# Optimization experiments

Hardware: AMD Instinct MI355X
Metric: run time of the kernel (lower is better)

Reference implementation:

```python
import jax, jax.numpy as jnp
import numpy as np

B, L, HID, H = 2, 2048, 1024, 16
HD = HID // H
MAX_REL = 2


def setup_inputs() -> dict:
    key = jax.random.key(0)
    ks = jax.random.split(key, 16)
    s = 0.02
    return {
        "query": jax.random.normal(ks[0], (B, L, HID), jnp.float32),
        "key": jax.random.normal(ks[1], (B, L, HID), jnp.float32),
        "value": jax.random.normal(ks[2], (B, L, HID), jnp.float32),
        "Wq": jax.random.normal(ks[3], (HID, HID), jnp.float32) * s,
        "bq": jnp.zeros((HID,), jnp.float32),
        "Wk": jax.random.normal(ks[4], (HID, HID), jnp.float32) * s,
        "bk": jnp.zeros((HID,), jnp.float32),
        "Wv": jax.random.normal(ks[5], (HID, HID), jnp.float32) * s,
        "bv": jnp.zeros((HID,), jnp.float32),
        "Wo": jax.random.normal(ks[6], (HID, HID), jnp.float32) * s,
        "bo": jnp.zeros((HID,), jnp.float32),
        "rel_k_table": jax.random.normal(ks[7], (2 * MAX_REL + 1, HD), jnp.float32) * s,
        "rel_v_table": jax.random.normal(ks[8], (2 * MAX_REL + 1, HD), jnp.float32) * s,
    }


def _rel_embeddings(table, len_q, len_k):
    # Shaw-style clipped relative position lookup -> [len_q, len_k, head_dim]
    dist = jnp.arange(len_k)[None, :] - jnp.arange(len_q)[:, None]
    idx = jnp.clip(dist, -MAX_REL, MAX_REL) + MAX_REL
    return table[idx]


def reference(query, key, value, Wq, bq, Wk, bk, Wv, bv, Wo, bo, rel_k_table, rel_v_table):
    b, lq, hid = query.shape
    lk = key.shape[1]
    q = (query @ Wq.T + bq).reshape(b, lq, H, HD)   # [b, lq, h, hd]
    k = (key @ Wk.T + bk).reshape(b, lk, H, HD)     # [b, lk, h, hd]
    v = (value @ Wv.T + bv).reshape(b, lk, H, HD)   # [b, lk, h, hd]

    rk = _rel_embeddings(rel_k_table, lq, lk)       # [lq, lk, hd]
    rv = _rel_embeddings(rel_v_table, lq, lk)       # [lq, lk, hd]

    attn1 = jnp.einsum('bqhd,bkhd->bhqk', q, k)
    attn2 = jnp.einsum('bqhd,qkd->bhqk', q, rk)
    # NOTE: original code averages the two scores and does NOT divide by sqrt(head_dim)
    attn = jax.nn.softmax((attn1 + attn2) * 0.5, axis=-1)

    w1 = jnp.einsum('bhqk,bkhd->bhqd', attn, v)
    w2 = jnp.einsum('bhqk,qkd->bhqd', attn, rv)
    x = (w1 + w2).transpose(0, 2, 1, 3).reshape(b, lq, hid)
    return x @ Wo.T + bo
```

## Files before the change

kernel.cpp:

```cpp
#include <hip/hip_runtime.h>
#include <hip/hip_bf16.h>
#include <math.h>

typedef __attribute__((ext_vector_type(8))) short bf16x8;
typedef __attribute__((ext_vector_type(4))) float f32x4;
typedef __attribute__((ext_vector_type(16))) float f32x16;

constexpr int Bc   = 2;
constexpr int Lc   = 2048;
constexpr int HIDc = 1024;
constexpr int Hc   = 16;
constexpr int HDc  = 64;
constexpr int Mc   = 4096;

__device__ __forceinline__ ushort f2bf(float f) {
  uint u = __float_as_uint(f);
  u += 0x7fff + ((u >> 16) & 1);
  return (ushort)(u >> 16);
}

__device__ __forceinline__ void gload16(const ushort* g, ushort* l) {
  __builtin_amdgcn_global_load_lds(
      (const __attribute__((address_space(1))) uint*)(const void*)g,
      (__attribute__((address_space(3))) uint*)(void*)l, 16, 0, 0);
}

__device__ __forceinline__ uint cvtpk(float lo, float hi_) {
  uint r;
  asm("v_cvt_pk_bf16_f32 %0, %1, %2" : "=v"(r) : "v"(lo), "v"(hi_));
  return r;
}
__device__ __forceinline__ void pswap(uint &a, uint &b) {
  asm("v_permlane32_swap_b32 %0, %1" : "+v"(a), "+v"(b));
}

template<int MODE>
__device__ __forceinline__ void gemm_core(
    const float* __restrict__ A, const float* __restrict__ Bw,
    const float* __restrict__ bias, float* __restrict__ Cf,
    ushort* __restrict__ Cb, int tile,
    ushort (*As)[2048], ushort (*Bs)[4096])
{
  const int tid  = threadIdx.x;
  const int lane = tid & 63;
  const int w    = tid >> 6;
  const int g    = lane >> 4;
  const int lc   = lane & 15;
  const int wr   = w >> 2;
  const int wc   = w & 3;
  const int row0 = (tile >> 3) * 64;
  const int col0 = (tile & 7) * 128;

  const int sr  = tid >> 2;
  const int sc_ = tid & 3;
  const int wofs = sr*32 + (sc_ ^ ((sr >> 1) & 3))*8;
  const float* pA = A  + (size_t)(row0 + sr) * HIDc + sc_*8;
  const float* pB = Bw + (size_t)(col0 + sr) * HIDc + sc_*8;

  int aoff[2], boff[2];
  #pragma unroll
  for (int mi = 0; mi < 2; ++mi) {
    int r = wr*32 + mi*16 + lc;
    aoff[mi] = r*32 + (g ^ ((r >> 1) & 3)) * 8;
  }
  #pragma unroll
  for (int ni = 0; ni < 2; ++ni) {
    int r = wc*32 + ni*16 + lc;
    boff[ni] = r*32 + (g ^ ((r >> 1) & 3)) * 8;
  }

  f32x4 acc[2][2];
  #pragma unroll
  for (int mi = 0; mi < 2; ++mi)
    #pragma unroll
    for (int ni = 0; ni < 2; ++ni) acc[mi][ni] = (f32x4){0.f,0.f,0.f,0.f};

  float4 a0, a1, b0, b1;
  auto ld = [&](int ko) {
    b0 = *(const float4*)(pB + ko);
    b1 = *(const float4*)(pB + ko + 4);
    if (tid < 256) {
      a0 = *(const float4*)(pA + ko);
      a1 = *(const float4*)(pA + ko + 4);
    }
  };
  auto wrbuf = [&](int bi) {
    ushort tb[8] = { f2bf(b0.x), f2bf(b0.y), f2bf(b0.z), f2bf(b0.w),
                     f2bf(b1.x), f2bf(b1.y), f2bf(b1.z), f2bf(b1.w) };
    *(uint4*)&Bs[bi][wofs] = *(uint4*)tb;
    if (tid < 256) {
      ushort ta[8] = { f2bf(a0.x), f2bf(a0.y), f2bf(a0.z), f2bf(a0.w),
                       f2bf(a1.x), f2bf(a1.y), f2bf(a1.z), f2bf(a1.w) };
      *(uint4*)&As[bi][wofs] = *(uint4*)ta;
    }
  };

  ld(0); wrbuf(0);
  __syncthreads();

  for (int t = 0; t < 32; ++t) {
    if (t < 31) ld((t + 1) * 32);
    const ushort* as = As[t & 1];
    const ushort* bs = Bs[t & 1];
    bf16x8 af[2], bfr[2];
    #pragma unroll
    for (int mi = 0; mi < 2; ++mi) af[mi] = *(const bf16x8*)&as[aoff[mi]];
    #pragma unroll
    for (int ni = 0; ni < 2; ++ni) bfr[ni] = *(const bf16x8*)&bs[boff[ni]];
    #pragma unroll
    for (int mi = 0; mi < 2; ++mi)
      #pragma unroll
      for (int ni = 0; ni < 2; ++ni)
        acc[mi][ni] = __builtin_amdgcn_mfma_f32_16x16x32_bf16(af[mi], bfr[ni], acc[mi][ni], 0, 0, 0);
    if (t < 31) wrbuf((t + 1) & 1);
    __syncthreads();
  }

  const int colbase = col0 + wc*32;
  if (MODE == 0) {
    #pragma unroll
    for (int mi = 0; mi < 2; ++mi) {
      int row = row0 + wr*32 + mi*16 + 4*g;
      #pragma unroll
      for (int ni = 0; ni < 2; ++ni) {
        int col = colbase + ni*16 + lc;
        float bb = bias[col];
        #pragma unroll
        for (int reg = 0; reg < 4; ++reg)
          Cf[(size_t)(row + reg) * HIDc + col] = acc[mi][ni][reg] + bb;
      }
    }
  } else if (MODE == 1) {
    #pragma unroll
    for (int mi = 0; mi < 2; ++mi) {
      int row = row0 + wr*32 + mi*16 + 4*g;
      int b = row >> 11, qq = row & 2047;
      #pragma unroll
      for (int ni = 0; ni < 2; ++ni) {
        int col = colbase + ni*16 + lc;
        int h = col >> 6, d = col & 63;
        float bb = bias[col];
        size_t base = (((size_t)b*Hc + h)*Lc + qq)*HDc + d;
        #pragma unroll
        for (int reg = 0; reg < 4; ++reg)
          Cb[base + (size_t)reg*HDc] = f2bf(acc[mi][ni][reg] + bb);
      }
    }
  } else {
    #pragma unroll
    for (int mi = 0; mi < 2; ++mi) {
      int row = row0 + wr*32 + mi*16 + 4*g;
      int b = row >> 11, kk = row & 2047;
      #pragma unroll
      for (int ni = 0; ni < 2; ++ni) {
        int col = colbase + ni*16 + lc;
        int h = col >> 6, d = col & 63;
        float bb = bias[col];
        ushort t4[4];
        #pragma unroll
        for (int reg = 0; reg < 4; ++reg) t4[reg] = f2bf(acc[mi][ni][reg] + bb);
        *(uint2*)&Cb[(((size_t)b*Hc + h)*HDc + d)*Lc + kk] = *(uint2*)t4;
      }
    }
  }
}

__global__ __launch_bounds__(512)
void gemm_fused(const float* __restrict__ q, const float* __restrict__ k,
                const float* __restrict__ v,
                const float* __restrict__ Wq, const float* __restrict__ Wk,
                const float* __restrict__ Wv,
                const float* __restrict__ bq, const float* __restrict__ bk,
                const float* __restrict__ bv,
                ushort* Qc, ushort* Kc, ushort* Vt)
{
  __shared__ ushort As[2][2048];
  __shared__ ushort Bs[2][4096];
  int gi   = blockIdx.x >> 9;
  int tile = blockIdx.x & 511;
  if (gi == 0)      gemm_core<1>(q, Wq, bq, nullptr, Qc, tile, As, Bs);
  else if (gi == 1) gemm_core<1>(k, Wk, bk, nullptr, Kc, tile, As, Bs);
  else              gemm_core<2>(v, Wv, bv, nullptr, Vt, tile, As, Bs);
}

__global__ __launch_bounds__(512)
void gemm_out(const float* __restrict__ X, const float* __restrict__ Wo,
              const float* __restrict__ bo, float* __restrict__ out)
{
  __shared__ ushort As[2][2048];
  __shared__ ushort Bs[2][4096];
  gemm_core<0>(X, Wo, bo, out, nullptr, blockIdx.x, As, Bs);
}

__global__ __launch_bounds__(128)
void attn_mfma32(const ushort* __restrict__ Qc, const ushort* __restrict__ Kc,
                 const ushort* __restrict__ Vt, const float* __restrict__ relk,
                 const float* __restrict__ relv, float* __restrict__ X)
{
  __shared__ ushort KVs[2][4608];

  const int tid  = threadIdx.x;
  const int w    = tid >> 6;
  const int lane = tid & 63;
  const int lq   = lane & 31;
  const int hi   = lane >> 5;

  const int swz  = (blockIdx.x & 7) * 128 + (blockIdx.x >> 3);
  const int qblk = swz & 31;
  const int bh   = swz >> 5;
  const int b    = bh >> 4;
  const int h    = bh & 15;
  const int qw   = qblk*64 + w*32;
  const int qabs = qw + lq;

  constexpr float C2 = 0.72134752f;

  const ushort* Kbh = Kc + (size_t)bh*Lc*HDc;
  const ushort* Vbh = Vt + (size_t)bh*HDc*Lc;

  bf16x8 qf[4];
  const ushort* qbase = Qc + ((size_t)bh*Lc + qabs)*HDc + 8*hi;
  #pragma unroll
  for (int s = 0; s < 4; ++s) qf[s] = *(const bf16x8*)(qbase + 16*s);

  f32x16 dc;
  #pragma unroll
  for (int i = 0; i < 16; ++i) dc[i] = 0.f;
  #pragma unroll
  for (int s = 0; s < 4; ++s) {
    union { ushort u[8]; bf16x8 v; } rf;
    #pragma unroll
    for (int j = 0; j < 8; ++j) rf.u[j] = 0;
    if (lq < 5) {
      #pragma unroll
      for (int j = 0; j < 8; ++j) rf.u[j] = f2bf(relk[lq*HDc + 16*s + 8*hi + j]);
    }
    dc = __builtin_amdgcn_mfma_f32_32x32x16_bf16(rf.v, qf[s], dc, 0, 0, 0);
  }
  float o0 = __shfl_xor(dc[0], 32), o1 = __shfl_xor(dc[1], 32),
        o2 = __shfl_xor(dc[2], 32), o3 = __shfl_xor(dc[3], 32);
  float dqh0, dqh1, dqh2, dqh3, dqh4;
  if (hi == 0) { dqh0 = dc[0]; dqh1 = dc[1]; dqh2 = dc[2]; dqh3 = dc[3]; dqh4 = o0; }
  else         { dqh0 = o0;    dqh1 = o1;    dqh2 = o2;    dqh3 = o3;    dqh4 = dc[0]; }
  dqh0 *= C2; dqh1 *= C2; dqh2 *= C2; dqh3 *= C2; dqh4 *= C2;

  f32x16 acc0, acc1;
  #pragma unroll
  for (int i = 0; i < 16; ++i) { acc0[i] = 0.f; acc1[i] = 0.f; }
  float lsum = 0.f, llo = 0.f, e1 = 0.f, e2 = 0.f, e3 = 0.f;

  auto stage = [&](ushort* dst, int k0) {
    #pragma unroll
    for (int seg = 0; seg < 5; ++seg) {
      int widx = seg*2 + w;
      if (widx < 5) {
        int vc = widx*64 + lane;
        int row = vc/5, ch = vc - row*5;
        gload16(Vbh + (size_t)row*Lc + k0 + ch*8, dst + vc*8);
      } else if (widx < 9) {
        int kc = (widx - 5)*64 + lane;
        int row = kc >> 3, pch = kc & 7;
        int gch = pch ^ (row & 7);
        gload16(Kbh + (size_t)(k0 + row)*HDc + gch*8, dst + (320 + kc)*8);
      }
    }
  };

  stage(KVs[0], 0);
  __syncthreads();

  for (int t = 0; t < Lc/32; ++t) {
    const ushort* vb_ = KVs[t & 1];
    const ushort* kb_ = vb_ + 2560;
    if (t + 1 < Lc/32) stage(KVs[(t+1) & 1], (t+1)*32);
    const int kb = t*32;

    bf16x8 kfa[4];
    #pragma unroll
    for (int s = 0; s < 4; ++s)
      kfa[s] = *(const bf16x8*)&kb_[lq*64 + ((2*s + hi) ^ (lq & 7))*8];
    f32x16 c0;
    #pragma unroll
    for (int i = 0; i < 16; ++i) c0[i] = 0.f;
    __builtin_amdgcn_s_setprio(1);
    #pragma unroll
    for (int s = 0; s < 4; ++s)
      c0 = __builtin_amdgcn_mfma_f32_32x32x16_bf16(kfa[s], qf[s], c0, 0, 0, 0);
    __builtin_amdgcn_s_setprio(0);

    bf16x8 vf00 = *(const bf16x8*)&vb_[lq*40      + hi*8];
    bf16x8 vf01 = *(const bf16x8*)&vb_[(32+lq)*40 + hi*8];
    bf16x8 vf10 = *(const bf16x8*)&vb_[lq*40      + (2+hi)*8];
    bf16x8 vf11 = *(const bf16x8*)&vb_[(32+lq)*40 + (2+hi)*8];

    uint pk[8];
    const bool allhi = (kb >= qw + 33);
    const bool alllo = (kb + 33 <= qw);
    if (allhi | alllo) {
      const float dq = allhi ? dqh4 : dqh0;
      float gs = 0.f;
      #pragma unroll
      for (int jj = 0; jj < 8; ++jj) {
        float pa = __builtin_amdgcn_exp2f(__builtin_fmaf(c0[2*jj],   C2, dq));
        float pb = __builtin_amdgcn_exp2f(__builtin_fmaf(c0[2*jj+1], C2, dq));
        gs += pa + pb;
        pk[jj] = cvtpk(pa, pb);
      }
      lsum += gs;
      if (alllo) llo += gs;
    } else {
      int bnum = kb + 4*hi - qabs;
      #pragma unroll
      for (int jj = 0; jj < 8; ++jj) {
        int r0 = 2*jj;
        int d0 = bnum + ((r0 & 3) + 8*(r0 >> 2));
        int d1 = d0 + 1;
        float dqa = d0 <= -2 ? dqh0 : (d0 >= 2 ? dqh4 :
                    (d0 == -1 ? dqh1 : (d0 == 0 ? dqh2 : dqh3)));
        float dqb = d1 <= -2 ? dqh0 : (d1 >= 2 ? dqh4 :
                    (d1 == -1 ? dqh1 : (d1 == 0 ? dqh2 : dqh3)));
        float pa = __builtin_amdgcn_exp2f(__builtin_fmaf(c0[r0],   C2, dqa));
        float pb = __builtin_amdgcn_exp2f(__builtin_fmaf(c0[r0+1], C2, dqb));
        lsum += pa + pb;
        llo += (d0 <= -2 ? pa : 0.f) + (d1 <= -2 ? pb : 0.f);
        e1  += (d0 == -1 ? pa : 0.f) + (d1 == -1 ? pb : 0.f);
        e2  += (d0 ==  0 ? pa : 0.f) + (d1 ==  0 ? pb : 0.f);
        e3  += (d0 ==  1 ? pa : 0.f) + (d1 ==  1 ? pb : 0.f);
        pk[jj] = cvtpk(pa, pb);
      }
    }

    uint X0 = pk[0], X1 = pk[1], Y0 = pk[2], Y1 = pk[3];
    pswap(X0, Y0); pswap(X1, Y1);
    union { uint u[4]; bf16x8 v; } aw0;
    aw0.u[0] = X0; aw0.u[1] = X1; aw0.u[2] = Y0; aw0.u[3] = Y1;
    X0 = pk[4]; X1 = pk[5]; Y0 = pk[6]; Y1 = pk[7];
    pswap(X0, Y0); pswap(X1, Y1);
    union { uint u[4]; bf16x8 v; } aw1;
    aw1.u[0] = X0; aw1.u[1] = X1; aw1.u[2] = Y0; aw1.u[3] = Y1;
    __builtin_amdgcn_s_setprio(1);
    acc0 = __builtin_amdgcn_mfma_f32_32x32x16_bf16(aw0.v, vf00, acc0, 0, 0, 0);
    acc1 = __builtin_amdgcn_mfma_f32_32x32x16_bf16(aw0.v, vf01, acc1, 0, 0, 0);
    acc0 = __builtin_amdgcn_mfma_f32_32x32x16_bf16(aw1.v, vf10, acc0, 0, 0, 0);
    acc1 = __builtin_amdgcn_mfma_f32_32x32x16_bf16(aw1.v, vf11, acc1, 0, 0, 0);
    __builtin_amdgcn_s_setprio(0);
    __syncthreads();
  }

  float Ls = lsum + __shfl_xor(lsum, 32);
  float Lo = llo  + __shfl_xor(llo, 32);
  float E1 = e1   + __shfl_xor(e1, 32);
  float E2 = e2   + __shfl_xor(e2, 32);
  float E3 = e3   + __shfl_xor(e3, 32);
  float inv = 1.f / Ls;
  float s0v = Lo*inv, s1v = E1*inv, s2v = E2*inv, s3v = E3*inv;
  float s4v = 1.f - s0v - s1v - s2v - s3v;

  float rvv[5][2];
  #pragma unroll
  for (int r = 0; r < 5; ++r) {
    rvv[r][0] = relv[r*HDc + lq];
    rvv[r][1] = relv[r*HDc + 32 + lq];
  }
  #pragma unroll
  for (int r = 0; r < 16; ++r) {
    int qloc = ((r & 3) + 8*(r >> 2)) + 4*hi;
    float iv = __shfl(inv, qloc);
    float t0 = __shfl(s0v, qloc);
    float t1 = __shfl(s1v, qloc);
    float t2 = __shfl(s2v, qloc);
    float t3 = __shfl(s3v, qloc);
    float t4 = __shfl(s4v, qloc);
    size_t rowb = ((size_t)(b*Lc + qw + qloc))*HIDc + h*HDc;
    X[rowb + lq]      = acc0[r]*iv + t0*rvv[0][0] + t1*rvv[1][0] + t2*rvv[2][0]
                      + t3*rvv[3][0] + t4*rvv[4][0];
    X[rowb + 32 + lq] = acc1[r]*iv + t0*rvv[0][1] + t1*rvv[1][1] + t2*rvv[2][1]
                      + t3*rvv[3][1] + t4*rvv[4][1];
  }
}

extern "C" void kernel_launch(void* const* d_in, const int* in_sizes, int n_in,
                              void* d_out, int out_size, void* d_ws, size_t ws_size,
                              hipStream_t stream) {
  const float* query = (const float*)d_in[0];
  const float* key   = (const float*)d_in[1];
  const float* value = (const float*)d_in[2];
  const float* Wq    = (const float*)d_in[3];
  const float* bq    = (const float*)d_in[4];
  const float* Wk    = (const float*)d_in[5];
  const float* bk    = (const float*)d_in[6];
  const float* Wv    = (const float*)d_in[7];
  const float* bv    = (const float*)d_in[8];
  const float* Wo    = (const float*)d_in[9];
  const float* bo    = (const float*)d_in[10];
  const float* relk  = (const float*)d_in[11];
  const float* relv  = (const float*)d_in[12];
  float* out = (float*)d_out;

  size_t S = (size_t)Bc * Hc * Lc * HDc;
  ushort* Qc = (ushort*)d_ws;
  ushort* Kc = Qc + S;
  ushort* Vt = Kc + S;
  float*  Xb = (float*)(Vt + S);

  gemm_fused<<<3*512, 512, 0, stream>>>(query, key, value, Wq, Wk, Wv,
                                        bq, bk, bv, Qc, Kc, Vt);

  attn_mfma32<<<Bc * Hc * (Lc / 64), 128, 0, stream>>>(Qc, Kc, Vt, relk, relv, Xb);

  gemm_out<<<512, 512, 0, stream>>>(Xb, Wo, bo, out);
}
```

Before: 178.4 us.

## Process two 32-row query groups per wave to reuse K/V tiles

Each wave in the attention kernel now handles 64 query rows as two 32-row groups, so the block covers 128 queries and the grid halves to 512 blocks. Every K/V tile staged in LDS and loaded into registers is reused by both groups. This halves global K/V traffic and LDS reads per query and gives more MFMA work per barrier. The cost is doubled accumulator and softmax-state registers, which may lower occupancy, and fewer blocks to spread across CUs.

```diff
diff --git a/kernel.cpp b/kernel.cpp
--- a/kernel.cpp
+++ b/kernel.cpp
@@ -205,27 +205,27 @@
   const int lq   = lane & 31;
   const int hi   = lane >> 5;
 
-  const int swz  = (blockIdx.x & 7) * 128 + (blockIdx.x >> 3);
-  const int qblk = swz & 31;
-  const int bh   = swz >> 5;
+  const int swz  = (blockIdx.x & 7) * 64 + (blockIdx.x >> 3);
+  const int qblk = swz & 15;
+  const int bh   = swz >> 4;
   const int b    = bh >> 4;
   const int h    = bh & 15;
-  const int qw   = qblk*64 + w*32;
-  const int qabs = qw + lq;
+  const int qw   = qblk*128 + w*64;
 
   constexpr float C2 = 0.72134752f;
 
   const ushort* Kbh = Kc + (size_t)bh*Lc*HDc;
   const ushort* Vbh = Vt + (size_t)bh*HDc*Lc;
 
-  bf16x8 qf[4];
-  const ushort* qbase = Qc + ((size_t)bh*Lc + qabs)*HDc + 8*hi;
-  #pragma unroll
-  for (int s = 0; s < 4; ++s) qf[s] = *(const bf16x8*)(qbase + 16*s);
-
-  f32x16 dc;
-  #pragma unroll
-  for (int i = 0; i < 16; ++i) dc[i] = 0.f;
+  bf16x8 qf[2][4];
+  #pragma unroll
+  for (int g = 0; g < 2; ++g) {
+    const ushort* qbase = Qc + ((size_t)bh*Lc + qw + 32*g + lq)*HDc + 8*hi;
+    #pragma unroll
+    for (int s = 0; s < 4; ++s) qf[g][s] = *(const bf16x8*)(qbase + 16*s);
+  }
+
+  bf16x8 rkf[4];
   #pragma unroll
   for (int s = 0; s < 4; ++s) {
     union { ushort u[8]; bf16x8 v; } rf;
@@ -235,19 +235,36 @@
       #pragma unroll
       for (int j = 0; j < 8; ++j) rf.u[j] = f2bf(relk[lq*HDc + 16*s + 8*hi + j]);
     }
-    dc = __builtin_amdgcn_mfma_f32_32x32x16_bf16(rf.v, qf[s], dc, 0, 0, 0);
-  }
-  float o0 = __shfl_xor(dc[0], 32), o1 = __shfl_xor(dc[1], 32),
-        o2 = __shfl_xor(dc[2], 32), o3 = __shfl_xor(dc[3], 32);
-  float dqh0, dqh1, dqh2, dqh3, dqh4;
-  if (hi == 0) { dqh0 = dc[0]; dqh1 = dc[1]; dqh2 = dc[2]; dqh3 = dc[3]; dqh4 = o0; }
-  else         { dqh0 = o0;    dqh1 = o1;    dqh2 = o2;    dqh3 = o3;    dqh4 = dc[0]; }
-  dqh0 *= C2; dqh1 *= C2; dqh2 *= C2; dqh3 *= C2; dqh4 *= C2;
-
-  f32x16 acc0, acc1;
-  #pragma unroll
-  for (int i = 0; i < 16; ++i) { acc0[i] = 0.f; acc1[i] = 0.f; }
-  float lsum = 0.f, llo = 0.f, e1 = 0.f, e2 = 0.f, e3 = 0.f;
+    rkf[s] = rf.v;
+  }
+
+  float dqh[2][5];
+  #pragma unroll
+  for (int g = 0; g < 2; ++g) {
+    f32x16 dc;
+    #pragma unroll
+    for (int i = 0; i < 16; ++i) dc[i] = 0.f;
+    #pragma unroll
+    for (int s = 0; s < 4; ++s)
+      dc = __builtin_amdgcn_mfma_f32_32x32x16_bf16(rkf[s], qf[g][s], dc, 0, 0, 0);
+    float o0 = __shfl_xor(dc[0], 32), o1 = __shfl_xor(dc[1], 32),
+          o2 = __shfl_xor(dc[2], 32), o3 = __shfl_xor(dc[3], 32);
+    if (hi == 0) { dqh[g][0] = dc[0]; dqh[g][1] = dc[1]; dqh[g][2] = dc[2];
+                   dqh[g][3] = dc[3]; dqh[g][4] = o0; }
+    else         { dqh[g][0] = o0;    dqh[g][1] = o1;    dqh[g][2] = o2;
+                   dqh[g][3] = o3;    dqh[g][4] = dc[0]; }
+    #pragma unroll
+    for (int r = 0; r < 5; ++r) dqh[g][r] *= C2;
+  }
+
+  f32x16 acc0[2], acc1[2];
+  float lsum[2], llo[2], e1[2], e2[2], e3[2];
+  #pragma unroll
+  for (int g = 0; g < 2; ++g) {
+    #pragma unroll
+    for (int i = 0; i < 16; ++i) { acc0[g][i] = 0.f; acc1[g][i] = 0.f; }
+    lsum[g] = llo[g] = e1[g] = e2[g] = e3[g] = 0.f;
+  }
 
   auto stage = [&](ushort* dst, int k0) {
     #pragma unroll
@@ -279,82 +296,78 @@
     #pragma unroll
     for (int s = 0; s < 4; ++s)
       kfa[s] = *(const bf16x8*)&kb_[lq*64 + ((2*s + hi) ^ (lq & 7))*8];
-    f32x16 c0;
-    #pragma unroll
-    for (int i = 0; i < 16; ++i) c0[i] = 0.f;
-    __builtin_amdgcn_s_setprio(1);
-    #pragma unroll
-    for (int s = 0; s < 4; ++s)
-      c0 = __builtin_amdgcn_mfma_f32_32x32x16_bf16(kfa[s], qf[s], c0, 0, 0, 0);
-    __builtin_amdgcn_s_setprio(0);
-
-    bf16x8 vf00 = *(const bf16x8*)&vb_[lq*40      + hi*8];
-    bf16x8 vf01 = *(const bf16x8*)&vb_[(32+lq)*40 + hi*8];
-    bf16x8 vf10 = *(const bf16x8*)&vb_[lq*40      + (2+hi)*8];
-    bf16x8 vf11 = *(const bf16x8*)&vb_[(32+lq)*40 + (2+hi)*8];
-
-    uint pk[8];
-    const bool allhi = (kb >= qw + 33);
-    const bool alllo = (kb + 33 <= qw);
-    if (allhi | alllo) {
-      const float dq = allhi ? dqh4 : dqh0;
-      float gs = 0.f;
-      #pragma unroll
-      for (int jj = 0; jj < 8; ++jj) {
-        float pa = __builtin_amdgcn_exp2f(__builtin_fmaf(c0[2*jj],   C2, dq));
-        float pb = __builtin_amdgcn_exp2f(__builtin_fmaf(c0[2*jj+1], C2, dq));
-        gs += pa + pb;
-        pk[jj] = cvtpk(pa, pb);
+    bf16x8 vf[4];
+    vf[0] = *(const bf16x8*)&vb_[lq*40      + hi*8];
+    vf[1] = *(const bf16x8*)&vb_[(32+lq)*40 + hi*8];
+    vf[2] = *(const bf16x8*)&vb_[lq*40      + (2+hi)*8];
+    vf[3] = *(const bf16x8*)&vb_[(32+lq)*40 + (2+hi)*8];
+
+    #pragma unroll
+    for (int g = 0; g < 2; ++g) {
+      const int qwg = qw + 32*g;
+      f32x16 c0;
+      #pragma unroll
+      for (int i = 0; i < 16; ++i) c0[i] = 0.f;
+      __builtin_amdgcn_s_setprio(1);
+      #pragma unroll
+      for (int s = 0; s < 4; ++s)
+        c0 = __builtin_amdgcn_mfma_f32_32x32x16_bf16(kfa[s], qf[g][s], c0, 0, 0, 0);
+      __builtin_amdgcn_s_setprio(0);
+
+      uint pk[8];
+      const bool allhi = (kb >= qwg + 33);
+      const bool alllo = (kb + 33 <= qwg);
+      if (allhi | alllo) {
+        const float dq = allhi ? dqh[g][4] : dqh[g][0];
+        float gs = 0.f;
+        #pragma unroll
+        for (int jj = 0; jj < 8; ++jj) {
+          float pa = __builtin_amdgcn_exp2f(__builtin_fmaf(c0[2*jj],   C2, dq));
+          float pb = __builtin_amdgcn_exp2f(__builtin_fmaf(c0[2*jj+1], C2, dq));
+          gs += pa + pb;
+          pk[jj] = cvtpk(pa, pb);
+        }
+        lsum[g] += gs;
+        if (alllo) llo[g] += gs;
+      } else {
+        int bnum = kb + 4*hi - (qwg + lq);
+        #pragma unroll
+        for (int jj = 0; jj < 8; ++jj) {
+          int r0 = 2*jj;
+          int d0 = bnum + ((r0 & 3) + 8*(r0 >> 2));
+          int d1 = d0 + 1;
+          float dqa = d0 <= -2 ? dqh[g][0] : (d0 >= 2 ? dqh[g][4] :
+                      (d0 == -1 ? dqh[g][1] : (d0 == 0 ? dqh[g][2] : dqh[g][3])));
+          float dqb = d1 <= -2 ? dqh[g][0] : (d1 >= 2 ? dqh[g][4] :
+                      (d1 == -1 ? dqh[g][1] : (d1 == 0 ? dqh[g][2] : dqh[g][3])));
+          float pa = __builtin_amdgcn_exp2f(__builtin_fmaf(c0[r0],   C2, dqa));
+          float pb = __builtin_amdgcn_exp2f(__builtin_fmaf(c0[r0+1], C2, dqb));
+          lsum[g] += pa + pb;
+          llo[g] += (d0 <= -2 ? pa : 0.f) + (d1 <= -2 ? pb : 0.f);
+          e1[g]  += (d0 == -1 ? pa : 0.f) + (d1 == -1 ? pb : 0.f);
+          e2[g]  += (d0 ==  0 ? pa : 0.f) + (d1 ==  0 ? pb : 0.f);
+          e3[g]  += (d0 ==  1 ? pa : 0.f) + (d1 ==  1 ? pb : 0.f);
+          pk[jj] = cvtpk(pa, pb);
+        }
       }
-      lsum += gs;
-      if (alllo) llo += gs;
-    } else {
-      int bnum = kb + 4*hi - qabs;
-      #pragma unroll
-      for (int jj = 0; jj < 8; ++jj) {
-        int r0 = 2*jj;
-        int d0 = bnum + ((r0 & 3) + 8*(r0 >> 2));
-        int d1 = d0 + 1;
-        float dqa = d0 <= -2 ? dqh0 : (d0 >= 2 ? dqh4 :
-                    (d0 == -1 ? dqh1 : (d0 == 0 ? dqh2 : dqh3)));
-        float dqb = d1 <= -2 ? dqh0 : (d1 >= 2 ? dqh4 :
-                    (d1 == -1 ? dqh1 : (d1 == 0 ? dqh2 : dqh3)));
-        float pa = __builtin_amdgcn_exp2f(__builtin_fmaf(c0[r0],   C2, dqa));
-        float pb = __builtin_amdgcn_exp2f(__builtin_fmaf(c0[r0+1], C2, dqb));
-        lsum += pa + pb;
-        llo += (d0 <= -2 ? pa : 0.f) + (d1 <= -2 ? pb : 0.f);
-        e1  += (d0 == -1 ? pa : 0.f) + (d1 == -1 ? pb : 0.f);
-        e2  += (d0 ==  0 ? pa : 0.f) + (d1 ==  0 ? pb : 0.f);
-        e3  += (d0 ==  1 ? pa : 0.f) + (d1 ==  1 ? pb : 0.f);
-        pk[jj] = cvtpk(pa, pb);
-      }
-    }
-
-    uint X0 = pk[0], X1 = pk[1], Y0 = pk[2], Y1 = pk[3];
-    pswap(X0, Y0); pswap(X1, Y1);
-    union { uint u[4]; bf16x8 v; } aw0;
-    aw0.u[0] = X0; aw0.u[1] = X1; aw0.u[2] = Y0; aw0.u[3] = Y1;
-    X0 = pk[4]; X1 = pk[5]; Y0 = pk[6]; Y1 = pk[7];
-    pswap(X0, Y0); pswap(X1, Y1);
-    union { uint u[4]; bf16x8 v; } aw1;
-    aw1.u[0] = X0; aw1.u[1] = X1; aw1.u[2] = Y0; aw1.u[3] = Y1;
-    __builtin_amdgcn_s_setprio(1);
-    acc0 = __builtin_amdgcn_mfma_f32_32x32x16_bf16(aw0.v, vf00, acc0, 0, 0, 0);
-    acc1 = __builtin_amdgcn_mfma_f32_32x32x16_bf16(aw0.v, vf01, acc1, 0, 0, 0);
-    acc0 = __builtin_amdgcn_mfma_f32_32x32x16_bf16(aw1.v, vf10, acc0, 0, 0, 0);
-    acc1 = __builtin_amdgcn_mfma_f32_32x32x16_bf16(aw1.v, vf11, acc1, 0, 0, 0);
-    __builtin_amdgcn_s_setprio(0);
+
+      uint X0 = pk[0], X1 = pk[1], Y0 = pk[2], Y1 = pk[3];
+      pswap(X0, Y0); pswap(X1, Y1);
+      union { uint u[4]; bf16x8 v; } aw0;
+      aw0.u[0] = X0; aw0.u[1] = X1; aw0.u[2] = Y0; aw0.u[3] = Y1;
+      X0 = pk[4]; X1 = pk[5]; Y0 = pk[6]; Y1 = pk[7];
+      pswap(X0, Y0); pswap(X1, Y1);
+      union { uint u[4]; bf16x8 v; } aw1;
+      aw1.u[0] = X0; aw1.u[1] = X1; aw1.u[2] = Y0; aw1.u[3] = Y1;
+      __builtin_amdgcn_s_setprio(1);
+      acc0[g] = __builtin_amdgcn_mfma_f32_32x32x16_bf16(aw0.v, vf[0], acc0[g], 0, 0, 0);
+      acc1[g] = __builtin_amdgcn_mfma_f32_32x32x16_bf16(aw0.v, vf[1], acc1[g], 0, 0, 0);
+      acc0[g] = __builtin_amdgcn_mfma_f32_32x32x16_bf16(aw1.v, vf[2], acc0[g], 0, 0, 0);
+      acc1[g] = __builtin_amdgcn_mfma_f32_32x32x16_bf16(aw1.v, vf[3], acc1[g], 0, 0, 0);
+      __builtin_amdgcn_s_setprio(0);
+    }
     __syncthreads();
   }
-
-  float Ls = lsum + __shfl_xor(lsum, 32);
-  float Lo = llo  + __shfl_xor(llo, 32);
-  float E1 = e1   + __shfl_xor(e1, 32);
-  float E2 = e2   + __shfl_xor(e2, 32);
-  float E3 = e3   + __shfl_xor(e3, 32);
-  float inv = 1.f / Ls;
-  float s0v = Lo*inv, s1v = E1*inv, s2v = E2*inv, s3v = E3*inv;
-  float s4v = 1.f - s0v - s1v - s2v - s3v;
 
   float rvv[5][2];
   #pragma unroll
@@ -363,19 +376,30 @@
     rvv[r][1] = relv[r*HDc + 32 + lq];
   }
   #pragma unroll
-  for (int r = 0; r < 16; ++r) {
-    int qloc = ((r & 3) + 8*(r >> 2)) + 4*hi;
-    float iv = __shfl(inv, qloc);
-    float t0 = __shfl(s0v, qloc);
-    float t1 = __shfl(s1v, qloc);
-    float t2 = __shfl(s2v, qloc);
-    float t3 = __shfl(s3v, qloc);
-    float t4 = __shfl(s4v, qloc);
-    size_t rowb = ((size_t)(b*Lc + qw + qloc))*HIDc + h*HDc;
-    X[rowb + lq]      = acc0[r]*iv + t0*rvv[0][0] + t1*rvv[1][0] + t2*rvv[2][0]
-                      + t3*rvv[3][0] + t4*rvv[4][0];
-    X[rowb + 32 + lq] = acc1[r]*iv + t0*rvv[0][1] + t1*rvv[1][1] + t2*rvv[2][1]
-                      + t3*rvv[3][1] + t4*rvv[4][1];
+  for (int g = 0; g < 2; ++g) {
+    float Ls = lsum[g] + __shfl_xor(lsum[g], 32);
+    float Lo = llo[g]  + __shfl_xor(llo[g], 32);
+    float E1 = e1[g]   + __shfl_xor(e1[g], 32);
+    float E2 = e2[g]   + __shfl_xor(e2[g], 32);
+    float E3 = e3[g]   + __shfl_xor(e3[g], 32);
+    float inv = 1.f / Ls;
+    float s0v = Lo*inv, s1v = E1*inv, s2v = E2*inv, s3v = E3*inv;
+    float s4v = 1.f - s0v - s1v - s2v - s3v;
+    #pragma unroll
+    for (int r = 0; r < 16; ++r) {
+      int qloc = ((r & 3) + 8*(r >> 2)) + 4*hi;
+      float iv = __shfl(inv, qloc);
+      float t0 = __shfl(s0v, qloc);
+      float t1 = __shfl(s1v, qloc);
+      float t2 = __shfl(s2v, qloc);
+      float t3 = __shfl(s3v, qloc);
+      float t4 = __shfl(s4v, qloc);
+      size_t rowb = ((size_t)(b*Lc + qw + 32*g + qloc))*HIDc + h*HDc;
+      X[rowb + lq]      = acc0[g][r]*iv + t0*rvv[0][0] + t1*rvv[1][0]
+                        + t2*rvv[2][0] + t3*rvv[3][0] + t4*rvv[4][0];
+      X[rowb + 32 + lq] = acc1[g][r]*iv + t0*rvv[0][1] + t1*rvv[1][1]
+                        + t2*rvv[2][1] + t3*rvv[3][1] + t4*rvv[4][1];
+    }
   }
 }
 
@@ -406,7 +430,7 @@
   gemm_fused<<<3*512, 512, 0, stream>>>(query, key, value, Wq, Wk, Wv,
                                         bq, bk, bv, Qc, Kc, Vt);
 
-  attn_mfma32<<<Bc * Hc * (Lc / 64), 128, 0, stream>>>(Qc, Kc, Vt, relk, relv, Xb);
+  attn_mfma32<<<512, 128, 0, stream>>>(Qc, Kc, Vt, relk, relv, Xb);
 
   gemm_out<<<512, 512, 0, stream>>>(Xb, Wo, bo, out);
 }
```

After: 193.5 us. 1.08x slower.
